# Performance work log

Measured on AMD Instinct MI355X. Metric: run time of the kernel, lower is better.

The kernel has to match this reference:

```python
import jax, jax.numpy as jnp
import numpy as np

DEGREE = 4  # sh degree -> DEGREE**2 = 16 components
RES = 128
N_PTS = 2097152
CH = 3


def sh_components(degree, d):
    """Real SH basis values for unit directions d [..., 3] -> [..., degree**2]."""
    x, y, z = d[..., 0], d[..., 1], d[..., 2]
    xx, yy, zz = x * x, y * y, z * z
    xy, yz, xz = x * y, y * z, x * z
    comps = [jnp.full(x.shape, 0.28209479177387814, dtype=d.dtype)]
    if degree > 1:
        comps += [-0.4886025119029199 * y,
                  0.4886025119029199 * z,
                  -0.4886025119029199 * x]
    if degree > 2:
        comps += [1.0925484305920792 * xy,
                  -1.0925484305920792 * yz,
                  0.31539156525252005 * (2.0 * zz - xx - yy),
                  -1.0925484305920792 * xz,
                  0.5462742152960396 * (xx - yy)]
    if degree > 3:
        comps += [-0.5900435899266435 * y * (3 * xx - yy),
                  2.890611442640554 * xy * z,
                  -0.4570457994644658 * y * (4 * zz - xx - yy),
                  0.3731763325901154 * z * (2 * zz - 3 * xx - 3 * yy),
                  -0.4570457994644658 * x * (4 * zz - xx - yy),
                  1.445305721320277 * z * (xx - yy),
                  -0.5900435899266435 * x * (xx - 3 * yy)]
    if degree > 4:
        comps += [2.5033429417967046 * xy * (xx - yy),
                  -1.7701307697799304 * yz * (3 * xx - yy),
                  0.9461746957575601 * xy * (7 * zz - 1),
                  -0.6690465435572892 * yz * (7 * zz - 3),
                  0.10578554691520431 * (zz * (35 * zz - 30) + 3),
                  -0.6690465435572892 * xz * (7 * zz - 3),
                  0.47308734787878004 * (xx - yy) * (7 * zz - 1),
                  -1.7701307697799304 * xz * (xx - 3 * yy),
                  0.6258357354491761 * (xx * (xx - 3 * yy) - yy * (3 * xx - yy))]
    return jnp.stack(comps, axis=-1)


def trilerp(coefficients, aabb, points):
    """Trilinear interpolation of grid coefficients [R,R,R,D2,C] at points [N,3] -> [N,D2,C]."""
    res = coefficients.shape[0]
    amin, amax = aabb[:3], aabb[3:]
    g = (points - amin) / (amax - amin) * (res - 1)       # continuous grid coords
    g = jnp.clip(g, 0.0, res - 1.0)
    i0 = jnp.clip(jnp.floor(g).astype(jnp.int32), 0, res - 2)  # [N,3]
    f = g - i0.astype(g.dtype)                            # fractional part [N,3]
    fx, fy, fz = f[..., 0], f[..., 1], f[..., 2]
    out = None
    for dx in (0, 1):
        wx = fx if dx else (1.0 - fx)
        for dy in (0, 1):
            wy = fy if dy else (1.0 - fy)
            for dz in (0, 1):
                wz = fz if dz else (1.0 - fz)
                w = (wx * wy * wz)[:, None, None]          # [N,1,1]
                c = coefficients[i0[:, 0] + dx, i0[:, 1] + dy, i0[:, 2] + dz]  # [N,D2,C]
                out = w * c if out is None else out + w * c
    return out


def setup_inputs() -> dict:
    key = jax.random.key(0)
    k1, k2, k3 = jax.random.split(key, 3)
    coefficients = jax.random.normal(k1, (RES, RES, RES, DEGREE ** 2, CH), dtype=jnp.float32) * 0.1
    aabb = jnp.array([-1.0, -1.0, -1.0, 1.0, 1.0, 1.0], dtype=jnp.float32)
    points = jax.random.uniform(k2, (N_PTS, 3), dtype=jnp.float32) * 2.0 - 1.0  # inside aabb
    normals = jax.random.normal(k3, (N_PTS, 3), dtype=jnp.float32)
    normals = normals / jnp.linalg.norm(normals, axis=-1, keepdims=True)
    return {"coefficients": coefficients, "aabb": aabb, "points": points, "normals": normals}


def reference(coefficients, aabb, points, normals):
    comps = sh_components(DEGREE, normals)                 # [N, D2]
    ic = trilerp(coefficients, aabb, points)               # [N, D2, C]
    irradiance = jnp.sum(ic * comps[..., None], axis=1)    # [N, C]
    return jnp.maximum(irradiance, 0.0)
```

## Files before the change

### kernel.cpp

```cpp
#include <hip/hip_runtime.h>


constexpr int RES = 128;
constexpr int D2 = 16;
constexpr int CSTRIDE = D2 * 3;
constexpr int CELL_F4 = CSTRIDE / 4;

constexpr int NBX = 32, NBY = 16, NBZ = 16;
constexpr int NBINS = NBX * NBY * NBZ;
constexpr int HX = 5, HY = 9, HZ = 9;
constexpr int MAIN_THREADS = 256;

constexpr int SRC_COL_F4 = HZ * CELL_F4;
constexpr int COL_F4 = SRC_COL_F4 + 1;
constexpr int NCOL = HX * HY;
constexpr int TOT_SRC_F4 = NCOL * SRC_COL_F4;
constexpr int LDS_F4 = NCOL * COL_F4;
constexpr int LOAD_ITERS = (TOT_SRC_F4 + MAIN_THREADS - 1) / MAIN_THREADS;

constexpr int REPL = 4;
constexpr int CAP = 104;
constexpr int CNT_PAD = 16;
constexpr int OVF_CAP = 131072;

__device__ __forceinline__ void grid_coords(const float* aabb, float px, float py, float pz,
                                            int& ix, int& iy, int& iz,
                                            float& fx, float& fy, float& fz)
{
    const float a0 = aabb[0], a1 = aabb[1], a2 = aabb[2];
    const float b0 = aabb[3], b1 = aabb[4], b2 = aabb[5];
    float gx = (px - a0) / (b0 - a0) * (float)(RES - 1);
    float gy = (py - a1) / (b1 - a1) * (float)(RES - 1);
    float gz = (pz - a2) / (b2 - a2) * (float)(RES - 1);
    gx = fminf(fmaxf(gx, 0.0f), (float)(RES - 1));
    gy = fminf(fmaxf(gy, 0.0f), (float)(RES - 1));
    gz = fminf(fmaxf(gz, 0.0f), (float)(RES - 1));
    ix = min((int)floorf(gx), RES - 2);
    iy = min((int)floorf(gy), RES - 2);
    iz = min((int)floorf(gz), RES - 2);
    fx = gx - (float)ix;
    fy = gy - (float)iy;
    fz = gz - (float)iz;
}

__device__ __forceinline__ int bin_of(int ix, int iy, int iz)
{
    return (((ix >> 2) * NBY) + (iy >> 3)) * NBZ + (iz >> 3);
}

__device__ __forceinline__ void sh_basis(float nx, float ny, float nz, float* sh)
{
    const float xx = nx * nx, yy = ny * ny, zz = nz * nz;
    const float xy = nx * ny, yz = ny * nz, xz = nx * nz;
    sh[0]  = 0.28209479177387814f;
    sh[1]  = -0.4886025119029199f * ny;
    sh[2]  = 0.4886025119029199f * nz;
    sh[3]  = -0.4886025119029199f * nx;
    sh[4]  = 1.0925484305920792f * xy;
    sh[5]  = -1.0925484305920792f * yz;
    sh[6]  = 0.31539156525252005f * (2.0f * zz - xx - yy);
    sh[7]  = -1.0925484305920792f * xz;
    sh[8]  = 0.5462742152960396f * (xx - yy);
    sh[9]  = -0.5900435899266435f * ny * (3.0f * xx - yy);
    sh[10] = 2.890611442640554f * xy * nz;
    sh[11] = -0.4570457994644658f * ny * (4.0f * zz - xx - yy);
    sh[12] = 0.3731763325901154f * nz * (2.0f * zz - 3.0f * xx - 3.0f * yy);
    sh[13] = -0.4570457994644658f * nx * (4.0f * zz - xx - yy);
    sh[14] = 1.445305721320277f * nz * (xx - yy);
    sh[15] = -0.5900435899266435f * nx * (xx - 3.0f * yy);
}

__device__ void compute_point_global(
    const float* __restrict__ coeff,
    const float* __restrict__ aabb,
    const float* __restrict__ points,
    const float* __restrict__ normals,
    float* __restrict__ out, int i)
{
    const float px = points[3 * i + 0], py = points[3 * i + 1], pz = points[3 * i + 2];
    const float nx = normals[3 * i + 0], ny = normals[3 * i + 1], nz = normals[3 * i + 2];
    int ix, iy, iz; float fx, fy, fz;
    grid_coords(aabb, px, py, pz, ix, iy, iz, fx, fy, fz);
    float sh[D2];
    sh_basis(nx, ny, nz, sh);
    const float wz0 = 1.0f - fz, wz1 = fz;
    float acc0 = 0.0f, acc1 = 0.0f, acc2 = 0.0f;
#pragma unroll
    for (int dx = 0; dx < 2; ++dx) {
        const float wx = dx ? fx : 1.0f - fx;
#pragma unroll
        for (int dy = 0; dy < 2; ++dy) {
            const float wxy = wx * (dy ? fy : 1.0f - fy);
            const int cell = (((ix + dx) * RES + (iy + dy)) * RES + iz) * CSTRIDE;
            const float4* __restrict__ cp = (const float4*)(coeff + cell);
            union { float4 q[24]; float v[96]; } u;
#pragma unroll
            for (int kk = 0; kk < 24; ++kk) u.q[kk] = cp[kk];
            float s00 = 0.f, s01 = 0.f, s02 = 0.f;
            float s10 = 0.f, s11 = 0.f, s12 = 0.f;
#pragma unroll
            for (int j = 0; j < D2; ++j) {
                const float s = sh[j];
                s00 = fmaf(s, u.v[3 * j + 0], s00);
                s01 = fmaf(s, u.v[3 * j + 1], s01);
                s02 = fmaf(s, u.v[3 * j + 2], s02);
                s10 = fmaf(s, u.v[48 + 3 * j + 0], s10);
                s11 = fmaf(s, u.v[48 + 3 * j + 1], s11);
                s12 = fmaf(s, u.v[48 + 3 * j + 2], s12);
            }
            const float w0 = wxy * wz0, w1 = wxy * wz1;
            acc0 = fmaf(w0, s00, fmaf(w1, s10, acc0));
            acc1 = fmaf(w0, s01, fmaf(w1, s11, acc1));
            acc2 = fmaf(w0, s02, fmaf(w1, s12, acc2));
        }
    }
    out[3 * i + 0] = fmaxf(acc0, 0.0f);
    out[3 * i + 1] = fmaxf(acc1, 0.0f);
    out[3 * i + 2] = fmaxf(acc2, 0.0f);
}

__global__ __launch_bounds__(256) void scatter_kernel(
    const float* __restrict__ aabb,
    const float* __restrict__ points,
    int* __restrict__ cnt_p,
    int* __restrict__ slots,
    int* __restrict__ ovf_cnt,
    int* __restrict__ ovf,
    int n)
{
    const int i = blockIdx.x * blockDim.x + threadIdx.x;
    if (i >= n) return;
    int ix, iy, iz; float fx, fy, fz;
    grid_coords(aabb, points[3 * i + 0], points[3 * i + 1], points[3 * i + 2],
                ix, iy, iz, fx, fy, fz);
    const int bin = bin_of(ix, iy, iz);
    const int rep = (i >> 6) & (REPL - 1);
    const int g = bin * REPL + rep;
    const int pos = atomicAdd(&cnt_p[g * CNT_PAD], 1);
    if (pos < CAP) {
        slots[g * CAP + pos] = i;
    } else {
        const int o = atomicAdd(&ovf_cnt[0], 1);
        if (o < OVF_CAP) ovf[o] = i;
        else ovf_cnt[1] = 1;
    }
}

__global__ __launch_bounds__(MAIN_THREADS) void main_kernel(
    const float* __restrict__ coeff,
    const float* __restrict__ aabb,
    const float* __restrict__ points,
    const float* __restrict__ normals,
    const int* __restrict__ cnt_p,
    const int* __restrict__ slots,
    const int* __restrict__ ovf_cnt,
    const int* __restrict__ ovf,
    float* __restrict__ out,
    int n)
{
    extern __shared__ char smem[];
    float4* lds4 = (float4*)smem;

    const int bin = blockIdx.x;
    const int tid = threadIdx.x;
    const bool ovf_block = (bin == 0);

    const int c0 = min(cnt_p[(bin * REPL + 0) * CNT_PAD], CAP);
    const int c1 = min(cnt_p[(bin * REPL + 1) * CNT_PAD], CAP);
    const int c2 = min(cnt_p[(bin * REPL + 2) * CNT_PAD], CAP);
    const int c3 = min(cnt_p[(bin * REPL + 3) * CNT_PAD], CAP);
    const int tot = c0 + c1 + c2 + c3;
    if (tot == 0 && !ovf_block) return;

    if (tot > 0) {
        const int bx = bin / (NBY * NBZ);
        const int by = (bin / NBZ) % NBY;
        const int bz = bin % NBZ;
        const int x0 = bx << 2;
        const int y0 = by << 3;
        const int z0 = bz << 3;

        const float4* __restrict__ coeff4 = (const float4*)coeff;

#pragma unroll
        for (int k = 0; k < LOAD_ITERS; ++k) {
            const int u = tid + k * MAIN_THREADS;
            if (u < TOT_SRC_F4) {
                int col = u / SRC_COL_F4;
                int rem = u - col * SRC_COL_F4;
                int cx = col / HY;
                int cy = col - cx * HY;
                int cz = rem / CELL_F4;
                int kk = rem - cz * CELL_F4;
                int xg = min(x0 + cx, RES - 1);
                int yg = min(y0 + cy, RES - 1);
                int zg = min(z0 + cz, RES - 1);
                lds4[col * COL_F4 + rem] = coeff4[((xg * RES + yg) * RES + zg) * CELL_F4 + kk];
            }
        }
        __syncthreads();

        for (int t = tid; t < tot; t += MAIN_THREADS) {
            int k = t, r = 0;
            if (k >= c0) { k -= c0; r = 1;
                if (k >= c1) { k -= c1; r = 2;
                    if (k >= c2) { k -= c2; r = 3; } } }
            const int i = slots[(bin * REPL + r) * CAP + k];

            const float px = points[3 * i + 0];
            const float py = points[3 * i + 1];
            const float pz = points[3 * i + 2];
            const float nx = normals[3 * i + 0];
            const float ny = normals[3 * i + 1];
            const float nz = normals[3 * i + 2];

            int ix, iy, iz; float fx, fy, fz;
            grid_coords(aabb, px, py, pz, ix, iy, iz, fx, fy, fz);
            const int lx = ix - x0, ly = iy - y0, lz = iz - z0;

            float sh[D2];
            sh_basis(nx, ny, nz, sh);

            const float wz0 = 1.0f - fz, wz1 = fz;
            float acc0 = 0.0f, acc1 = 0.0f, acc2 = 0.0f;

#pragma unroll
            for (int dx = 0; dx < 2; ++dx) {
                const float wx = dx ? fx : 1.0f - fx;
#pragma unroll
                for (int dy = 0; dy < 2; ++dy) {
                    const float wxy = wx * (dy ? fy : 1.0f - fy);
                    const int lbase = ((lx + dx) * HY + (ly + dy)) * COL_F4 + lz * CELL_F4;
                    union { float4 q[24]; float v[96]; } u;
#pragma unroll
                    for (int kk = 0; kk < 24; ++kk) u.q[kk] = lds4[lbase + kk];

                    float s00 = 0.f, s01 = 0.f, s02 = 0.f;
                    float s10 = 0.f, s11 = 0.f, s12 = 0.f;
#pragma unroll
                    for (int j = 0; j < D2; ++j) {
                        const float s = sh[j];
                        s00 = fmaf(s, u.v[3 * j + 0], s00);
                        s01 = fmaf(s, u.v[3 * j + 1], s01);
                        s02 = fmaf(s, u.v[3 * j + 2], s02);
                        s10 = fmaf(s, u.v[48 + 3 * j + 0], s10);
                        s11 = fmaf(s, u.v[48 + 3 * j + 1], s11);
                        s12 = fmaf(s, u.v[48 + 3 * j + 2], s12);
                    }
                    const float w0 = wxy * wz0, w1 = wxy * wz1;
                    acc0 = fmaf(w0, s00, fmaf(w1, s10, acc0));
                    acc1 = fmaf(w0, s01, fmaf(w1, s11, acc1));
                    acc2 = fmaf(w0, s02, fmaf(w1, s12, acc2));
                }
            }

            out[3 * i + 0] = fmaxf(acc0, 0.0f);
            out[3 * i + 1] = fmaxf(acc1, 0.0f);
            out[3 * i + 2] = fmaxf(acc2, 0.0f);
        }
    }

    if (ovf_block) {
        const int m = min(ovf_cnt[0], OVF_CAP);
        for (int t = tid; t < m; t += MAIN_THREADS)
            compute_point_global(coeff, aabb, points, normals, out, ovf[t]);

        if (ovf_cnt[1]) {
            for (int i = tid; i < n; i += MAIN_THREADS) {
                int ix, iy, iz; float fx, fy, fz;
                grid_coords(aabb, points[3 * i + 0], points[3 * i + 1], points[3 * i + 2],
                            ix, iy, iz, fx, fy, fz);
                const int g = bin_of(ix, iy, iz) * REPL + ((i >> 6) & (REPL - 1));
                const int c = min(cnt_p[g * CNT_PAD], CAP);
                bool placed = false;
                for (int k = 0; k < c && !placed; ++k) placed = (slots[g * CAP + k] == i);
                for (int k = 0; k < m && !placed; ++k)  placed = (ovf[k] == i);
                if (!placed) compute_point_global(coeff, aabb, points, normals, out, i);
            }
        }
    }
}

__global__ __launch_bounds__(256) void direct_kernel(
    const float* __restrict__ coeff,
    const float* __restrict__ aabb,
    const float* __restrict__ points,
    const float* __restrict__ normals,
    float* __restrict__ out,
    int n)
{
    const int i = blockIdx.x * blockDim.x + threadIdx.x;
    if (i >= n) return;
    compute_point_global(coeff, aabb, points, normals, out, i);
}

extern "C" void kernel_launch(void* const* d_in, const int* in_sizes, int n_in,
                              void* d_out, int out_size, void* d_ws, size_t ws_size,
                              hipStream_t stream) {
    const float* coeff   = (const float*)d_in[0];
    const float* aabb    = (const float*)d_in[1];
    const float* points  = (const float*)d_in[2];
    const float* normals = (const float*)d_in[3];
    float* out = (float*)d_out;

    const int n = in_sizes[2] / 3;
    const int nblk = (n + 255) / 256;

    size_t off = 0;
    auto take = [&](size_t bytes) { size_t o = off; off = (off + bytes + 255) & ~(size_t)255; return o; };
    char* ws = (char*)d_ws;
    const size_t cnt_bytes = (size_t)NBINS * REPL * CNT_PAD * 4;
    const size_t o_cnt   = take(cnt_bytes);
    const size_t o_ovfc  = take(256);
    const size_t o_slots = take((size_t)NBINS * REPL * CAP * 4);
    const size_t o_ovf   = take((size_t)OVF_CAP * 4);
    const size_t needed = off;

    if (ws_size < needed) {
        hipLaunchKernelGGL(direct_kernel, dim3(nblk), dim3(256), 0, stream,
                           coeff, aabb, points, normals, out, n);
        return;
    }

    int* cnt_p   = (int*)(ws + o_cnt);
    int* ovf_cnt = (int*)(ws + o_ovfc);
    int* slots   = (int*)(ws + o_slots);
    int* ovf     = (int*)(ws + o_ovf);

    hipMemsetAsync(ws + o_cnt, 0, cnt_bytes + 256, stream);

    hipLaunchKernelGGL(scatter_kernel, dim3(nblk), dim3(256), 0, stream,
                       aabb, points, cnt_p, slots, ovf_cnt, ovf, n);
    hipLaunchKernelGGL(main_kernel, dim3(NBINS), dim3(MAIN_THREADS),
                       LDS_F4 * sizeof(float4), stream,
                       coeff, aabb, points, normals, cnt_p, slots, ovf_cnt, ovf, out, n);
}
```

Baseline: 794.8 us.

## Bin points per chunk in LDS and store packed point records

Replaces global-atomic binning with per-chunk binning: each scatter block counts bins in shared memory and writes packed position+normal+index records into per-(bin,chunk) slots, with byte counts per chunk. The main kernel builds a prefix sum over chunk counts and binary-searches it to find each record, reading the packed record instead of gathering points and normals by index. This is meant to remove global atomic contention and the random gathers in the main kernel. In exchange it uses more workspace and adds per-point search overhead, and the small per-chunk capacity may push more points to the slow overflow path.

```diff
diff --git a/kernel.cpp b/kernel.cpp
--- a/kernel.cpp
+++ b/kernel.cpp
@@ -9,18 +9,18 @@
 constexpr int NBX = 32, NBY = 16, NBZ = 16;
 constexpr int NBINS = NBX * NBY * NBZ;
 constexpr int HX = 5, HY = 9, HZ = 9;
-constexpr int MAIN_THREADS = 256;
 
 constexpr int SRC_COL_F4 = HZ * CELL_F4;
 constexpr int COL_F4 = SRC_COL_F4 + 1;
 constexpr int NCOL = HX * HY;
 constexpr int TOT_SRC_F4 = NCOL * SRC_COL_F4;
 constexpr int LDS_F4 = NCOL * COL_F4;
+constexpr int MAIN_THREADS = 256;
 constexpr int LOAD_ITERS = (TOT_SRC_F4 + MAIN_THREADS - 1) / MAIN_THREADS;
 
-constexpr int REPL = 4;
-constexpr int CAP = 104;
-constexpr int CNT_PAD = 16;
+constexpr int MAXCHUNK = 512;
+constexpr int CHUNK_PTS0 = 4096;
+constexpr int CAPC = 8;
 constexpr int OVF_CAP = 131072;
 
 __device__ __forceinline__ void grid_coords(const float* aabb, float px, float py, float pz,
@@ -70,6 +70,56 @@
     sh[15] = -0.5900435899266435f * nx * (xx - 3.0f * yy);
 }
 
+__device__ __forceinline__ void eval_from_lds(
+    const float4* __restrict__ lds4, const float* __restrict__ aabb,
+    float px, float py, float pz, float nx, float ny, float nz,
+    int x0, int y0, int z0, int i, float* __restrict__ out)
+{
+    int ix, iy, iz; float fx, fy, fz;
+    grid_coords(aabb, px, py, pz, ix, iy, iz, fx, fy, fz);
+    const int lx = ix - x0, ly = iy - y0, lz = iz - z0;
+
+    float sh[D2];
+    sh_basis(nx, ny, nz, sh);
+
+    const float wz0 = 1.0f - fz, wz1 = fz;
+    float acc0 = 0.0f, acc1 = 0.0f, acc2 = 0.0f;
+
+#pragma unroll
+    for (int dx = 0; dx < 2; ++dx) {
+        const float wx = dx ? fx : 1.0f - fx;
+#pragma unroll
+        for (int dy = 0; dy < 2; ++dy) {
+            const float wxy = wx * (dy ? fy : 1.0f - fy);
+            const int lbase = ((lx + dx) * HY + (ly + dy)) * COL_F4 + lz * CELL_F4;
+            union { float4 q[24]; float v[96]; } u;
+#pragma unroll
+            for (int kk = 0; kk < 24; ++kk) u.q[kk] = lds4[lbase + kk];
+
+            float s00 = 0.f, s01 = 0.f, s02 = 0.f;
+            float s10 = 0.f, s11 = 0.f, s12 = 0.f;
+#pragma unroll
+            for (int j = 0; j < D2; ++j) {
+                const float s = sh[j];
+                s00 = fmaf(s, u.v[3 * j + 0], s00);
+                s01 = fmaf(s, u.v[3 * j + 1], s01);
+                s02 = fmaf(s, u.v[3 * j + 2], s02);
+                s10 = fmaf(s, u.v[48 + 3 * j + 0], s10);
+                s11 = fmaf(s, u.v[48 + 3 * j + 1], s11);
+                s12 = fmaf(s, u.v[48 + 3 * j + 2], s12);
+            }
+            const float w0 = wxy * wz0, w1 = wxy * wz1;
+            acc0 = fmaf(w0, s00, fmaf(w1, s10, acc0));
+            acc1 = fmaf(w0, s01, fmaf(w1, s11, acc1));
+            acc2 = fmaf(w0, s02, fmaf(w1, s12, acc2));
+        }
+    }
+
+    out[3 * i + 0] = fmaxf(acc0, 0.0f);
+    out[3 * i + 1] = fmaxf(acc1, 0.0f);
+    out[3 * i + 2] = fmaxf(acc2, 0.0f);
+}
+
 __device__ void compute_point_global(
     const float* __restrict__ coeff,
     const float* __restrict__ aabb,
@@ -122,28 +172,44 @@
 __global__ __launch_bounds__(256) void scatter_kernel(
     const float* __restrict__ aabb,
     const float* __restrict__ points,
-    int* __restrict__ cnt_p,
-    int* __restrict__ slots,
+    const float* __restrict__ normals,
+    float4* __restrict__ slots4,
+    unsigned char* __restrict__ cnt8,
     int* __restrict__ ovf_cnt,
     int* __restrict__ ovf,
-    int n)
-{
-    const int i = blockIdx.x * blockDim.x + threadIdx.x;
-    if (i >= n) return;
-    int ix, iy, iz; float fx, fy, fz;
-    grid_coords(aabb, points[3 * i + 0], points[3 * i + 1], points[3 * i + 2],
-                ix, iy, iz, fx, fy, fz);
-    const int bin = bin_of(ix, iy, iz);
-    const int rep = (i >> 6) & (REPL - 1);
-    const int g = bin * REPL + rep;
-    const int pos = atomicAdd(&cnt_p[g * CNT_PAD], 1);
-    if (pos < CAP) {
-        slots[g * CAP + pos] = i;
-    } else {
-        const int o = atomicAdd(&ovf_cnt[0], 1);
-        if (o < OVF_CAP) ovf[o] = i;
-        else ovf_cnt[1] = 1;
-    }
+    int n, int nchunk, int chunk_pts)
+{
+    __shared__ int scnt[NBINS];
+    const int c = blockIdx.x;
+    const int tid = threadIdx.x;
+
+    for (int j = tid; j < NBINS; j += 256) scnt[j] = 0;
+    __syncthreads();
+
+    const int base = c * chunk_pts;
+    const int limit = min(chunk_pts, n - base);
+    for (int k = tid; k < limit; k += 256) {
+        const int i = base + k;
+        const float px = points[3 * i + 0], py = points[3 * i + 1], pz = points[3 * i + 2];
+        int ix, iy, iz; float fx, fy, fz;
+        grid_coords(aabb, px, py, pz, ix, iy, iz, fx, fy, fz);
+        const int bin = bin_of(ix, iy, iz);
+        const int pos = atomicAdd(&scnt[bin], 1);
+        if (pos < CAPC) {
+            const float nx = normals[3 * i + 0], ny = normals[3 * i + 1], nz = normals[3 * i + 2];
+            const size_t rec = ((size_t)bin * nchunk + c) * CAPC + pos;
+            slots4[rec * 2 + 0] = make_float4(px, py, pz, nx);
+            slots4[rec * 2 + 1] = make_float4(ny, nz, __int_as_float(i), 0.0f);
+        } else {
+            const int o = atomicAdd(&ovf_cnt[0], 1);
+            if (o < OVF_CAP) ovf[o] = i;
+            else ovf_cnt[1] = 1;
+        }
+    }
+    __syncthreads();
+
+    for (int j = tid; j < NBINS; j += 256)
+        cnt8[(size_t)c * NBINS + j] = (unsigned char)min(scnt[j], CAPC);
 }
 
 __global__ __launch_bounds__(MAIN_THREADS) void main_kernel(
@@ -151,35 +217,49 @@
     const float* __restrict__ aabb,
     const float* __restrict__ points,
     const float* __restrict__ normals,
-    const int* __restrict__ cnt_p,
-    const int* __restrict__ slots,
+    const unsigned char* __restrict__ cnt8,
+    const float4* __restrict__ slots4,
     const int* __restrict__ ovf_cnt,
     const int* __restrict__ ovf,
     float* __restrict__ out,
-    int n)
+    int n, int nchunk, int chunk_pts)
 {
     extern __shared__ char smem[];
     float4* lds4 = (float4*)smem;
+    __shared__ int pref[MAXCHUNK + 1];
+    __shared__ int wsum[4];
 
     const int bin = blockIdx.x;
     const int tid = threadIdx.x;
-    const bool ovf_block = (bin == 0);
-
-    const int c0 = min(cnt_p[(bin * REPL + 0) * CNT_PAD], CAP);
-    const int c1 = min(cnt_p[(bin * REPL + 1) * CNT_PAD], CAP);
-    const int c2 = min(cnt_p[(bin * REPL + 2) * CNT_PAD], CAP);
-    const int c3 = min(cnt_p[(bin * REPL + 3) * CNT_PAD], CAP);
-    const int tot = c0 + c1 + c2 + c3;
-    if (tot == 0 && !ovf_block) return;
+    const bool ovfb = (bin == 0);
+
+    const int c0i = 2 * tid, c1i = 2 * tid + 1;
+    int cc0 = (c0i < nchunk) ? (int)cnt8[(size_t)c0i * NBINS + bin] : 0;
+    int cc1 = (c1i < nchunk) ? (int)cnt8[(size_t)c1i * NBINS + bin] : 0;
+    int s = cc0 + cc1;
+    const int lane = tid & 63, wv = tid >> 6;
+    for (int d = 1; d < 64; d <<= 1) {
+        int v = __shfl_up(s, d, 64);
+        if (lane >= d) s += v;
+    }
+    if (lane == 63) wsum[wv] = s;
+    __syncthreads();
+    int woff = 0;
+    for (int w = 0; w < wv; ++w) woff += wsum[w];
+    const int incl = s + woff;
+    pref[c0i] = incl - cc1 - cc0;
+    pref[c1i] = incl - cc1;
+    if (tid == 255) pref[MAXCHUNK] = incl;
+    __syncthreads();
+    const int tot = pref[MAXCHUNK];
+
+    if (tot == 0 && !ovfb) return;
 
     if (tot > 0) {
         const int bx = bin / (NBY * NBZ);
         const int by = (bin / NBZ) % NBY;
         const int bz = bin % NBZ;
-        const int x0 = bx << 2;
-        const int y0 = by << 3;
-        const int z0 = bz << 3;
-
+        const int x0 = bx << 2, y0 = by << 3, z0 = bz << 3;
         const float4* __restrict__ coeff4 = (const float4*)coeff;
 
 #pragma unroll
@@ -200,67 +280,23 @@
         }
         __syncthreads();
 
+        const int hi_end = min(nchunk, MAXCHUNK);
         for (int t = tid; t < tot; t += MAIN_THREADS) {
-            int k = t, r = 0;
-            if (k >= c0) { k -= c0; r = 1;
-                if (k >= c1) { k -= c1; r = 2;
-                    if (k >= c2) { k -= c2; r = 3; } } }
-            const int i = slots[(bin * REPL + r) * CAP + k];
-
-            const float px = points[3 * i + 0];
-            const float py = points[3 * i + 1];
-            const float pz = points[3 * i + 2];
-            const float nx = normals[3 * i + 0];
-            const float ny = normals[3 * i + 1];
-            const float nz = normals[3 * i + 2];
-
-            int ix, iy, iz; float fx, fy, fz;
-            grid_coords(aabb, px, py, pz, ix, iy, iz, fx, fy, fz);
-            const int lx = ix - x0, ly = iy - y0, lz = iz - z0;
-
-            float sh[D2];
-            sh_basis(nx, ny, nz, sh);
-
-            const float wz0 = 1.0f - fz, wz1 = fz;
-            float acc0 = 0.0f, acc1 = 0.0f, acc2 = 0.0f;
-
-#pragma unroll
-            for (int dx = 0; dx < 2; ++dx) {
-                const float wx = dx ? fx : 1.0f - fx;
-#pragma unroll
-                for (int dy = 0; dy < 2; ++dy) {
-                    const float wxy = wx * (dy ? fy : 1.0f - fy);
-                    const int lbase = ((lx + dx) * HY + (ly + dy)) * COL_F4 + lz * CELL_F4;
-                    union { float4 q[24]; float v[96]; } u;
-#pragma unroll
-                    for (int kk = 0; kk < 24; ++kk) u.q[kk] = lds4[lbase + kk];
-
-                    float s00 = 0.f, s01 = 0.f, s02 = 0.f;
-                    float s10 = 0.f, s11 = 0.f, s12 = 0.f;
-#pragma unroll
-                    for (int j = 0; j < D2; ++j) {
-                        const float s = sh[j];
-                        s00 = fmaf(s, u.v[3 * j + 0], s00);
-                        s01 = fmaf(s, u.v[3 * j + 1], s01);
-                        s02 = fmaf(s, u.v[3 * j + 2], s02);
-                        s10 = fmaf(s, u.v[48 + 3 * j + 0], s10);
-                        s11 = fmaf(s, u.v[48 + 3 * j + 1], s11);
-                        s12 = fmaf(s, u.v[48 + 3 * j + 2], s12);
-                    }
-                    const float w0 = wxy * wz0, w1 = wxy * wz1;
-                    acc0 = fmaf(w0, s00, fmaf(w1, s10, acc0));
-                    acc1 = fmaf(w0, s01, fmaf(w1, s11, acc1));
-                    acc2 = fmaf(w0, s02, fmaf(w1, s12, acc2));
-                }
-            }
-
-            out[3 * i + 0] = fmaxf(acc0, 0.0f);
-            out[3 * i + 1] = fmaxf(acc1, 0.0f);
-            out[3 * i + 2] = fmaxf(acc2, 0.0f);
-        }
-    }
-
-    if (ovf_block) {
+            int a = 0, b = hi_end;
+            while (b - a > 1) {
+                const int m = (a + b) >> 1;
+                if (pref[m] <= t) a = m; else b = m;
+            }
+            const int pos = t - pref[a];
+            const size_t rec = ((size_t)bin * nchunk + a) * CAPC + pos;
+            const float4 lo4 = slots4[rec * 2 + 0];
+            const float4 hi4 = slots4[rec * 2 + 1];
+            eval_from_lds(lds4, aabb, lo4.x, lo4.y, lo4.z, lo4.w, hi4.x, hi4.y,
+                          x0, y0, z0, __float_as_int(hi4.z), out);
+        }
+    }
+
+    if (ovfb) {
         const int m = min(ovf_cnt[0], OVF_CAP);
         for (int t = tid; t < m; t += MAIN_THREADS)
             compute_point_global(coeff, aabb, points, normals, out, ovf[t]);
@@ -270,11 +306,15 @@
                 int ix, iy, iz; float fx, fy, fz;
                 grid_coords(aabb, points[3 * i + 0], points[3 * i + 1], points[3 * i + 2],
                             ix, iy, iz, fx, fy, fz);
-                const int g = bin_of(ix, iy, iz) * REPL + ((i >> 6) & (REPL - 1));
-                const int c = min(cnt_p[g * CNT_PAD], CAP);
+                const int b2 = bin_of(ix, iy, iz);
+                const int ch = i / chunk_pts;
+                const int c = (int)cnt8[(size_t)ch * NBINS + b2];
                 bool placed = false;
-                for (int k = 0; k < c && !placed; ++k) placed = (slots[g * CAP + k] == i);
-                for (int k = 0; k < m && !placed; ++k)  placed = (ovf[k] == i);
+                for (int k = 0; k < c && !placed; ++k) {
+                    const size_t rec = ((size_t)b2 * nchunk + ch) * CAPC + k;
+                    placed = (__float_as_int(slots4[rec * 2 + 1].z) == i);
+                }
+                for (int k = 0; k < m && !placed; ++k) placed = (ovf[k] == i);
                 if (!placed) compute_point_global(coeff, aabb, points, normals, out, i);
             }
         }
@@ -304,34 +344,39 @@
     float* out = (float*)d_out;
 
     const int n = in_sizes[2] / 3;
-    const int nblk = (n + 255) / 256;
-
-    size_t off = 0;
-    auto take = [&](size_t bytes) { size_t o = off; off = (off + bytes + 255) & ~(size_t)255; return o; };
     char* ws = (char*)d_ws;
-    const size_t cnt_bytes = (size_t)NBINS * REPL * CNT_PAD * 4;
-    const size_t o_cnt   = take(cnt_bytes);
-    const size_t o_ovfc  = take(256);
-    const size_t o_slots = take((size_t)NBINS * REPL * CAP * 4);
-    const size_t o_ovf   = take((size_t)OVF_CAP * 4);
-    const size_t needed = off;
-
-    if (ws_size < needed) {
+
+    int nchunk = (n + CHUNK_PTS0 - 1) / CHUNK_PTS0;
+    if (nchunk > MAXCHUNK) nchunk = MAXCHUNK;
+    if (nchunk < 1) nchunk = 1;
+    const int chunk_pts = (n + nchunk - 1) / nchunk;
+
+    const size_t ovfc_bytes = 256;
+    const size_t ovf_bytes  = (size_t)OVF_CAP * 4;
+    const size_t cnt_bytes  = ((size_t)nchunk * NBINS + 255) & ~(size_t)255;
+    const size_t slot_bytes = (size_t)NBINS * nchunk * CAPC * 32;
+    const size_t need = ovfc_bytes + ovf_bytes + cnt_bytes + slot_bytes;
+
+    if (ws_size < need) {
+        const int nblk = (n + 255) / 256;
         hipLaunchKernelGGL(direct_kernel, dim3(nblk), dim3(256), 0, stream,
                            coeff, aabb, points, normals, out, n);
         return;
     }
 
-    int* cnt_p   = (int*)(ws + o_cnt);
-    int* ovf_cnt = (int*)(ws + o_ovfc);
-    int* slots   = (int*)(ws + o_slots);
-    int* ovf     = (int*)(ws + o_ovf);
-
-    hipMemsetAsync(ws + o_cnt, 0, cnt_bytes + 256, stream);
-
-    hipLaunchKernelGGL(scatter_kernel, dim3(nblk), dim3(256), 0, stream,
-                       aabb, points, cnt_p, slots, ovf_cnt, ovf, n);
+    int*           ovf_cnt = (int*)(ws);
+    int*           ovf     = (int*)(ws + ovfc_bytes);
+    unsigned char* cnt8    = (unsigned char*)(ws + ovfc_bytes + ovf_bytes);
+    float4*        slots4  = (float4*)(ws + ovfc_bytes + ovf_bytes + cnt_bytes);
+
+    hipMemsetAsync(ovf_cnt, 0, ovfc_bytes, stream);
+
+    hipLaunchKernelGGL(scatter_kernel, dim3(nchunk), dim3(256), 0, stream,
+                       aabb, points, normals, slots4, cnt8, ovf_cnt, ovf,
+                       n, nchunk, chunk_pts);
+
     hipLaunchKernelGGL(main_kernel, dim3(NBINS), dim3(MAIN_THREADS),
                        LDS_F4 * sizeof(float4), stream,
-                       coeff, aabb, points, normals, cnt_p, slots, ovf_cnt, ovf, out, n);
-}
+                       coeff, aabb, points, normals, cnt8, slots4, ovf_cnt, ovf, out,
+                       n, nchunk, chunk_pts);
+}
```

Measured after the change: 787.8 us. Within noise of the previous version (-0.9%).
